# Kernel tuning notes

Hardware: AMD Instinct MI355X
Metric: run time of the kernel (lower is better)

Reference implementation:

```python
import jax, jax.numpy as jnp
import numpy as np

WH, WW = 16, 16          # window size
NUM_HEADS = 6
DIM = 192
N = WH * WW              # tokens per window

def _rel_coords_table():
    # (2*WH-1, 2*WW-1, 2), normalized and scaled by 8 (Swin-V2 style)
    rch = np.arange(-(WH - 1), WH, dtype=np.float32)
    rcw = np.arange(-(WW - 1), WW, dtype=np.float32)
    tab = np.stack(np.meshgrid(rch, rcw, indexing='ij'), axis=-1)
    tab[..., 0] /= (WH - 1)
    tab[..., 1] /= (WW - 1)
    tab *= 8.0
    return tab

def _rel_pos_index():
    # (N, N) int indices into the flattened bias table
    coords = np.stack(np.meshgrid(np.arange(WH), np.arange(WW), indexing='ij'))  # (2,WH,WW)
    cf = coords.reshape(2, -1)                                                   # (2,N)
    rel = cf[:, :, None] - cf[:, None, :]                                        # (2,N,N)
    rel = rel.transpose(1, 2, 0).astype(np.int64)                                # (N,N,2)
    rel[..., 0] += WH - 1
    rel[..., 1] += WW - 1
    rel[..., 0] *= 2 * WW - 1
    return rel.sum(-1)                                                           # (N,N)

_TABLE = jnp.asarray(_rel_coords_table())          # (2WH-1, 2WW-1, 2)
_INDEX = jnp.asarray(_rel_pos_index().reshape(-1)) # (N*N,)

def setup_inputs() -> dict:
    key = jax.random.key(0)
    ks = jax.random.split(key, 8)
    B_ = 256  # num_windows(64) * batch(4)
    return {
        'x': jax.random.normal(ks[0], (B_, N, DIM), dtype=jnp.float32),
        'scale': jax.random.uniform(ks[1], (1, 2), dtype=jnp.float32),
        'mask': jnp.zeros((64, N, N), dtype=jnp.float32),
        'qkv_w': jax.random.normal(ks[2], (3 * DIM, DIM), dtype=jnp.float32) * 0.02,
        'qkv_b': jnp.zeros((3 * DIM,), dtype=jnp.float32),
        'cpb_w1': jax.random.normal(ks[3], (512, 4), dtype=jnp.float32) * 0.02,
        'cpb_b1': jnp.zeros((512,), dtype=jnp.float32),
        'cpb_w2': jax.random.normal(ks[4], (NUM_HEADS, 512), dtype=jnp.float32) * 0.02,
        'cpb_b2': jnp.zeros((NUM_HEADS,), dtype=jnp.float32),
        'proj_w': jax.random.normal(ks[5], (DIM, DIM), dtype=jnp.float32) * 0.02,
        'proj_b': jnp.zeros((DIM,), dtype=jnp.float32),
    }

def reference(x, scale, mask, qkv_w, qkv_b, cpb_w1, cpb_b1, cpb_w2, cpb_b2, proj_w, proj_b):
    B_, n, C = x.shape
    H = NUM_HEADS
    hd = C // H
    qk_scale = hd ** -0.5

    qkv = x @ qkv_w.T + qkv_b                       # (B_, N, 3C)
    qkv = qkv.reshape(B_, n, 3, H, hd).transpose(2, 0, 3, 1, 4)
    q, k, v = qkv[0], qkv[1], qkv[2]                # each (B_, H, N, hd)

    attn = jnp.einsum('bhnd,bhmd->bhnm', q * qk_scale, k)  # (B_, H, N, N)

    # continuous relative position bias: concat table with broadcast scale -> MLP
    rel_cell = jnp.broadcast_to(scale[0], _TABLE.shape[:2] + (2,))    # (2WH-1,2WW-1,2)
    coords4 = jnp.concatenate([_TABLE, rel_cell], axis=-1)            # (...,4)
    hmid = jax.nn.relu(coords4 @ cpb_w1.T + cpb_b1)                   # (...,512)
    table = (hmid @ cpb_w2.T + cpb_b2).reshape(-1, H)                 # (M, H)
    bias = table[_INDEX].reshape(n, n, H).transpose(2, 0, 1)          # (H, N, N)

    attn = attn + bias[None]
    nW = mask.shape[0]
    attn = attn.reshape(B_ // nW, nW, H, n, n) + mask[None, :, None]
    attn = attn.reshape(B_, H, n, n)
    attn = jax.nn.softmax(attn, axis=-1)

    out = jnp.einsum('bhnm,bhmd->bhnd', attn, v)    # (B_, H, N, hd)
    out = out.transpose(0, 2, 1, 3).reshape(B_, n, C)
    return out @ proj_w.T + proj_b
```

## Files before the change

### kernel.cpp

```cpp
#include <hip/hip_runtime.h>
#include <math.h>

#define N_TOK 256
#define NHEADS 6
#define DIM_C 192
#define HD 32
#define B_WIN 256

typedef short bf16x8 __attribute__((ext_vector_type(8)));
typedef float f32x4 __attribute__((ext_vector_type(4)));

__device__ inline short f2bf(float f) {
    unsigned u = __float_as_uint(f);
    u = (u + 0x7fffu + ((u >> 16) & 1u)) >> 16;
    return (short)u;
}
__device__ inline short f2bf_fast(float f) {
    return (short)((__float_as_uint(f) + 0x8000u) >> 16);
}
__device__ inline float bf2f(short s) {
    return __uint_as_float(((unsigned)(unsigned short)s) << 16);
}

__global__ __launch_bounds__(512) void cpb_table_kernel(
    const float* __restrict__ scale, const float* __restrict__ w1,
    const float* __restrict__ b1, const float* __restrict__ w2,
    const float* __restrict__ b2, float* __restrict__ table)
{
    __shared__ float red[512];
    const int e = blockIdx.x;
    const int i = e / 31, j = e % 31;
    const float t0 = ((float)(i - 15)) * (8.0f / 15.0f);
    const float t1 = ((float)(j - 15)) * (8.0f / 15.0f);
    const float s0 = scale[0], s1 = scale[1];
    const int t = threadIdx.x;
    const float* w = w1 + t * 4;
    float h = w[0] * t0 + w[1] * t1 + w[2] * s0 + w[3] * s1 + b1[t];
    h = fmaxf(h, 0.0f);
    for (int head = 0; head < NHEADS; ++head) {
        red[t] = h * w2[head * 512 + t];
        __syncthreads();
        for (int s = 256; s > 0; s >>= 1) {
            if (t < s) red[t] += red[t + s];
            __syncthreads();
        }
        if (t == 0) table[e * NHEADS + head] = red[0] + b2[head];
        __syncthreads();
    }
}


__global__ __launch_bounds__(256) void bias_perm_kernel(
    const float* __restrict__ table, short* __restrict__ bias_p)
{
    const int idx8 = blockIdx.x * 256 + threadIdx.x;
    const int h = idx8 >> 13;
    const int rem = idx8 & 8191;
    const int rb = rem >> 9;
    const int g = (rem >> 6) & 7;
    const int lane = rem & 63;
    const int quad = lane >> 4, l15 = lane & 15;
    bf16x8 o;
#pragma unroll
    for (int j = 0; j < 8; ++j) {
        const int nt = g * 2 + (j >> 2), r = j & 3;
        const int row = rb * 16 + quad * 4 + r;
        const int col = nt * 16 + l15;
        const int rel0 = (row >> 4) - (col >> 4) + 15;
        const int rel1 = (row & 15) - (col & 15) + 15;
        o[j] = f2bf(table[(rel0 * 31 + rel1) * NHEADS + h]);
    }
    ((bf16x8*)bias_p)[idx8] = o;
}

__global__ __launch_bounds__(256) void mask_perm_kernel(
    const float* __restrict__ mask, short* __restrict__ mask_p)
{
    const int idx8 = blockIdx.x * 256 + threadIdx.x;
    const int bw = idx8 >> 13;
    const int rem = idx8 & 8191;
    const int rb = rem >> 9;
    const int g = (rem >> 6) & 7;
    const int lane = rem & 63;
    const int quad = lane >> 4, l15 = lane & 15;
    const float* ms = mask + ((size_t)bw << 16);
    bf16x8 o;
#pragma unroll
    for (int j = 0; j < 8; ++j) {
        const int nt = g * 2 + (j >> 2), r = j & 3;
        const int row = rb * 16 + quad * 4 + r;
        const int col = nt * 16 + l15;
        o[j] = f2bf(ms[row * 256 + col]);
    }
    ((bf16x8*)mask_p)[idx8] = o;
}

__global__ __launch_bounds__(256) void f32_to_bf16_kernel(
    const float* __restrict__ in, short* __restrict__ out, int n4)
{
    const int i = blockIdx.x * 256 + threadIdx.x;
    if (i < n4) {
        float4 v = ((const float4*)in)[i];
        short4 s;
        s.x = f2bf(v.x); s.y = f2bf(v.y); s.z = f2bf(v.z); s.w = f2bf(v.w);
        ((short4*)out)[i] = s;
    }
}

__global__ __launch_bounds__(256) void qkv_gemm_kernel(
    const short* __restrict__ x16, const short* __restrict__ w16,
    const float* __restrict__ qkv_b,
    short* __restrict__ qb, short* __restrict__ kb, short* __restrict__ vb)
{
    const int t = threadIdx.x;
    const int lane = t & 63;
    const int w = t >> 6;
    const int l15 = lane & 15, quad = lane >> 4;
    const int n0 = blockIdx.x * 64;
    const int m0 = blockIdx.y * 128 + w * 32;

    f32x4 acc[2][4] = {};
#pragma unroll
    for (int ks = 0; ks < 6; ++ks) {
        bf16x8 af[2];
#pragma unroll
        for (int mt = 0; mt < 2; ++mt)
            af[mt] = *(const bf16x8*)(x16 + (size_t)(m0 + mt * 16 + l15) * DIM_C + ks * 32 + quad * 8);
        bf16x8 bfr[4];
#pragma unroll
        for (int nt = 0; nt < 4; ++nt)
            bfr[nt] = *(const bf16x8*)(w16 + (size_t)(n0 + nt * 16 + l15) * DIM_C + ks * 32 + quad * 8);
#pragma unroll
        for (int mt = 0; mt < 2; ++mt)
#pragma unroll
            for (int nt = 0; nt < 4; ++nt)
                acc[mt][nt] = __builtin_amdgcn_mfma_f32_16x16x32_bf16(af[mt], bfr[nt], acc[mt][nt], 0, 0, 0);
    }

    const int which = n0 / DIM_C;
    short* outp = (which == 0) ? qb : (which == 1) ? kb : vb;
    const float qscale = (which == 0) ? 0.17677669529663689f : 1.0f;
#pragma unroll
    for (int mt = 0; mt < 2; ++mt) {
#pragma unroll
        for (int r = 0; r < 4; ++r) {
            const int m = m0 + mt * 16 + quad * 4 + r;
            const int b = m >> 8, tok = m & 255;
#pragma unroll
            for (int nt = 0; nt < 4; ++nt) {
                const int c = n0 + nt * 16 + l15;
                const int rem = c - which * DIM_C;
                const int h = rem >> 5, d = rem & 31;
                const float val = (acc[mt][nt][r] + qkv_b[c]) * qscale;
                outp[((size_t)((b * NHEADS + h) * N_TOK + tok)) * HD + d] = f2bf(val);
            }
        }
    }
}

__global__ __launch_bounds__(256) void proj_gemm_kernel(
    const short* __restrict__ A16, const short* __restrict__ w16,
    const float* __restrict__ proj_b, float* __restrict__ out)
{
    const int t = threadIdx.x;
    const int lane = t & 63;
    const int w = t >> 6;
    const int l15 = lane & 15, quad = lane >> 4;
    const int n0 = blockIdx.x * 64;
    const int m0 = blockIdx.y * 128 + w * 32;

    f32x4 acc[2][4] = {};
#pragma unroll
    for (int ks = 0; ks < 6; ++ks) {
        bf16x8 af[2];
#pragma unroll
        for (int mt = 0; mt < 2; ++mt)
            af[mt] = *(const bf16x8*)(A16 + (size_t)(m0 + mt * 16 + l15) * DIM_C + ks * 32 + quad * 8);
        bf16x8 bfr[4];
#pragma unroll
        for (int nt = 0; nt < 4; ++nt)
            bfr[nt] = *(const bf16x8*)(w16 + (size_t)(n0 + nt * 16 + l15) * DIM_C + ks * 32 + quad * 8);
#pragma unroll
        for (int mt = 0; mt < 2; ++mt)
#pragma unroll
            for (int nt = 0; nt < 4; ++nt)
                acc[mt][nt] = __builtin_amdgcn_mfma_f32_16x16x32_bf16(af[mt], bfr[nt], acc[mt][nt], 0, 0, 0);
    }

#pragma unroll
    for (int mt = 0; mt < 2; ++mt) {
#pragma unroll
        for (int r = 0; r < 4; ++r) {
            const int m = m0 + mt * 16 + quad * 4 + r;
#pragma unroll
            for (int nt = 0; nt < 4; ++nt) {
                const int c = n0 + nt * 16 + l15;
                out[(size_t)m * DIM_C + c] = acc[mt][nt][r] + proj_b[c];
            }
        }
    }
}

#define PS_LD 264

__global__ __launch_bounds__(256, 3) void attn_mfma_kernel(
    const short* __restrict__ q, const short* __restrict__ k,
    const short* __restrict__ v, const short* __restrict__ bias_p,
    const short* __restrict__ mask_p, short* __restrict__ out16)
{
    __shared__ __align__(16) short Vt[32][PS_LD];
    __shared__ __align__(16) short Pw[4][16][PS_LD];

    const int h = blockIdx.x;
    const int b = blockIdx.y;
    const int t = threadIdx.x;
    const int lane = t & 63;
    const int w = t >> 6;
    const int l15 = lane & 15;
    const int quad = lane >> 4;
    const size_t slab = ((size_t)(b * NHEADS + h)) * (N_TOK * HD);

    {
        const bf16x8* vrow = (const bf16x8*)(v + slab + (size_t)t * HD);
#pragma unroll
        for (int u = 0; u < 4; ++u) {
            bf16x8 vv = vrow[u];
#pragma unroll
            for (int j = 0; j < 8; ++j) {
                const int d = u * 8 + j;
                Vt[d][t ^ (((d >> 3) & 1) * 16)] = vv[j];
            }
        }
    }
    __syncthreads();

    const short* bslab = bias_p + h * 65536;
    const short* mslab = mask_p + ((b & 63) * 65536);

    for (int chunk = 0; chunk < 4; ++chunk) {
        const int rb = chunk * 4 + w;

        const bf16x8 qf = *(const bf16x8*)(q + slab + (size_t)(rb * 16 + l15) * HD + quad * 8);

        f32x4 S[16];
#pragma unroll
        for (int nt = 0; nt < 16; ++nt) {
            const bf16x8 kf = *(const bf16x8*)(k + slab + (size_t)(nt * 16 + l15) * HD + quad * 8);
            f32x4 z = {0.f, 0.f, 0.f, 0.f};
            S[nt] = __builtin_amdgcn_mfma_f32_16x16x32_bf16(qf, kf, z, 0, 0, 0);
        }

        float mx[4] = {-1e30f, -1e30f, -1e30f, -1e30f};
#pragma unroll
        for (int half = 0; half < 2; ++half) {
            bf16x8 bb[4], mm[4];
#pragma unroll
            for (int gg = 0; gg < 4; ++gg) {
                const int g = half * 4 + gg;
                const int off = ((rb * 8 + g) * 64 + lane) * 8;
                bb[gg] = *(const bf16x8*)(bslab + off);
                mm[gg] = *(const bf16x8*)(mslab + off);
            }
#pragma unroll
            for (int gg = 0; gg < 4; ++gg) {
#pragma unroll
                for (int jj = 0; jj < 8; ++jj) {
                    const int nt = (half * 4 + gg) * 2 + (jj >> 2);
                    const int r = jj & 3;
                    const float sv = S[nt][r] + bf2f(bb[gg][jj]) + bf2f(mm[gg][jj]);
                    S[nt][r] = sv;
                    mx[r] = fmaxf(mx[r], sv);
                }
            }
        }

#pragma unroll
        for (int r = 0; r < 4; ++r) {
            mx[r] = fmaxf(mx[r], __shfl_xor(mx[r], 1));
            mx[r] = fmaxf(mx[r], __shfl_xor(mx[r], 2));
            mx[r] = fmaxf(mx[r], __shfl_xor(mx[r], 4));
            mx[r] = fmaxf(mx[r], __shfl_xor(mx[r], 8));
        }

        float sm[4] = {0.f, 0.f, 0.f, 0.f};
#pragma unroll
        for (int nt = 0; nt < 16; ++nt) {
#pragma unroll
            for (int r = 0; r < 4; ++r) {
                const float p = __expf(S[nt][r] - mx[r]);
                sm[r] += p;
                const int lr = quad * 4 + r;
                Pw[w][lr][(nt * 16 + l15) ^ (((lr >> 3) & 1) * 16)] = f2bf_fast(p);
            }
        }
        float inv[4];
#pragma unroll
        for (int r = 0; r < 4; ++r) {
            sm[r] += __shfl_xor(sm[r], 1);
            sm[r] += __shfl_xor(sm[r], 2);
            sm[r] += __shfl_xor(sm[r], 4);
            sm[r] += __shfl_xor(sm[r], 8);
            inv[r] = __builtin_amdgcn_rcpf(sm[r]);
        }

        __asm__ volatile("s_waitcnt lgkmcnt(0)" ::: "memory");

        f32x4 O0 = {0.f, 0.f, 0.f, 0.f};
        f32x4 O1 = {0.f, 0.f, 0.f, 0.f};
        const int sw = ((l15 >> 3) & 1) * 16;
#pragma unroll
        for (int ks = 0; ks < 8; ++ks) {
            const int cb = ks * 32 + quad * 8;
            bf16x8 af  = *(const bf16x8*)&Pw[w][l15][cb ^ sw];
            bf16x8 bf0 = *(const bf16x8*)&Vt[l15][cb ^ sw];
            bf16x8 bf1 = *(const bf16x8*)&Vt[16 + l15][cb ^ sw];
            O0 = __builtin_amdgcn_mfma_f32_16x16x32_bf16(af, bf0, O0, 0, 0, 0);
            O1 = __builtin_amdgcn_mfma_f32_16x16x32_bf16(af, bf1, O1, 0, 0, 0);
        }

#pragma unroll
        for (int r = 0; r < 4; ++r) {
            const int token = rb * 16 + quad * 4 + r;
            short* dst = out16 + ((size_t)(b * N_TOK + token)) * DIM_C + h * HD;
            dst[l15]      = f2bf_fast(O0[r] * inv[r]);
            dst[16 + l15] = f2bf_fast(O1[r] * inv[r]);
        }
    }
}

extern "C" void kernel_launch(void* const* d_in, const int* in_sizes, int n_in,
                              void* d_out, int out_size, void* d_ws, size_t ws_size,
                              hipStream_t stream)
{
    const float* x      = (const float*)d_in[0];
    const float* scale  = (const float*)d_in[1];
    const float* mask   = (const float*)d_in[2];
    const float* qkv_w  = (const float*)d_in[3];
    const float* qkv_b  = (const float*)d_in[4];
    const float* cpb_w1 = (const float*)d_in[5];
    const float* cpb_b1 = (const float*)d_in[6];
    const float* cpb_w2 = (const float*)d_in[7];
    const float* cpb_b2 = (const float*)d_in[8];
    const float* proj_w = (const float*)d_in[9];
    const float* proj_b = (const float*)d_in[10];
    float* out = (float*)d_out;

    const size_t per = (size_t)B_WIN * NHEADS * N_TOK * HD;
    short* wss     = (short*)d_ws;
    short* qb      = wss;
    short* kb      = qb + per;
    short* vb      = kb + per;
    short* ao      = vb + per;
    short* x16     = ao + per;
    short* bias_p  = x16 + per;
    short* mask_p  = bias_p + 393216;
    short* qkvw16  = mask_p + 4194304;
    short* projw16 = qkvw16 + 110592;
    float* table   = (float*)(projw16 + 36864);

    cpb_table_kernel<<<961, 512, 0, stream>>>(scale, cpb_w1, cpb_b1, cpb_w2, cpb_b2, table);

    bias_perm_kernel<<<(NHEADS * 8192) / 256, 256, 0, stream>>>(table, bias_p);
    mask_perm_kernel<<<(64 * 8192) / 256, 256, 0, stream>>>(mask, mask_p);

    f32_to_bf16_kernel<<<(int)((per / 4 + 255) / 256), 256, 0, stream>>>(x, x16, (int)(per / 4));
    f32_to_bf16_kernel<<<(110592 / 4 + 255) / 256, 256, 0, stream>>>(qkv_w, qkvw16, 110592 / 4);
    f32_to_bf16_kernel<<<(36864 / 4 + 255) / 256, 256, 0, stream>>>(proj_w, projw16, 36864 / 4);

    qkv_gemm_kernel<<<dim3(9, 512), 256, 0, stream>>>(x16, qkvw16, qkv_b, qb, kb, vb);

    attn_mfma_kernel<<<dim3(NHEADS, B_WIN), 256, 0, stream>>>(qb, kb, vb, bias_p, mask_p, ao);

    proj_gemm_kernel<<<dim3(3, 512), 256, 0, stream>>>(ao, projw16, proj_b, out);
}
```

Measured before the change: 361.8 us.

## Hoist K fragments, fold bias+mask into MFMA accumulator, remap blocks for mask reuse

The attention kernel now loads all 16 K fragments into registers once per block instead of once per row chunk. The bias and mask sum is passed as the MFMA accumulator input, which removes a separate add pass. The grid is flattened, and blocks are remapped so that consecutive blocks share the same mask window across heads and batches, which should improve L2 reuse. The cost is higher register pressure from holding 16 K fragments, which may lower occupancy under launch_bounds(256,3).

```diff
diff --git a/kernel.cpp b/kernel.cpp
--- a/kernel.cpp
+++ b/kernel.cpp
@@ -211,8 +211,13 @@
     __shared__ __align__(16) short Vt[32][PS_LD];
     __shared__ __align__(16) short Pw[4][16][PS_LD];
 
-    const int h = blockIdx.x;
-    const int b = blockIdx.y;
+    const int l = blockIdx.x;
+    const int s = l >> 3;
+    const int bw = (l & 7) + 8 * (s / 24);
+    const int j = s % 24;
+    const int h = j % 6;
+    const int b = (j / 6) * 64 + bw;
+
     const int t = threadIdx.x;
     const int lane = t & 63;
     const int w = t >> 6;
@@ -226,16 +231,22 @@
         for (int u = 0; u < 4; ++u) {
             bf16x8 vv = vrow[u];
 #pragma unroll
-            for (int j = 0; j < 8; ++j) {
-                const int d = u * 8 + j;
-                Vt[d][t ^ (((d >> 3) & 1) * 16)] = vv[j];
-            }
-        }
-    }
+            for (int jj = 0; jj < 8; ++jj) {
+                const int d = u * 8 + jj;
+                Vt[d][t ^ (((d >> 3) & 1) * 16)] = vv[jj];
+            }
+        }
+    }
+
+    bf16x8 kfr[16];
+#pragma unroll
+    for (int nt = 0; nt < 16; ++nt)
+        kfr[nt] = *(const bf16x8*)(k + slab + (size_t)(nt * 16 + l15) * HD + quad * 8);
+
     __syncthreads();
 
     const short* bslab = bias_p + h * 65536;
-    const short* mslab = mask_p + ((b & 63) * 65536);
+    const short* mslab = mask_p + bw * 65536;
 
     for (int chunk = 0; chunk < 4; ++chunk) {
         const int rb = chunk * 4 + w;
@@ -243,14 +254,6 @@
         const bf16x8 qf = *(const bf16x8*)(q + slab + (size_t)(rb * 16 + l15) * HD + quad * 8);
 
         f32x4 S[16];
-#pragma unroll
-        for (int nt = 0; nt < 16; ++nt) {
-            const bf16x8 kf = *(const bf16x8*)(k + slab + (size_t)(nt * 16 + l15) * HD + quad * 8);
-            f32x4 z = {0.f, 0.f, 0.f, 0.f};
-            S[nt] = __builtin_amdgcn_mfma_f32_16x16x32_bf16(qf, kf, z, 0, 0, 0);
-        }
-
-        float mx[4] = {-1e30f, -1e30f, -1e30f, -1e30f};
 #pragma unroll
         for (int half = 0; half < 2; ++half) {
             bf16x8 bb[4], mm[4];
@@ -263,17 +266,24 @@
             }
 #pragma unroll
             for (int gg = 0; gg < 4; ++gg) {
-#pragma unroll
-                for (int jj = 0; jj < 8; ++jj) {
-                    const int nt = (half * 4 + gg) * 2 + (jj >> 2);
-                    const int r = jj & 3;
-                    const float sv = S[nt][r] + bf2f(bb[gg][jj]) + bf2f(mm[gg][jj]);
-                    S[nt][r] = sv;
-                    mx[r] = fmaxf(mx[r], sv);
+                const int g = half * 4 + gg;
+                f32x4 c0, c1;
+#pragma unroll
+                for (int r = 0; r < 4; ++r) {
+                    c0[r] = bf2f(bb[gg][r])     + bf2f(mm[gg][r]);
+                    c1[r] = bf2f(bb[gg][4 + r]) + bf2f(mm[gg][4 + r]);
                 }
-            }
-        }
-
+                S[g * 2]     = __builtin_amdgcn_mfma_f32_16x16x32_bf16(qf, kfr[g * 2],     c0, 0, 0, 0);
+                S[g * 2 + 1] = __builtin_amdgcn_mfma_f32_16x16x32_bf16(qf, kfr[g * 2 + 1], c1, 0, 0, 0);
+            }
+        }
+
+        float mx[4] = {-1e30f, -1e30f, -1e30f, -1e30f};
+#pragma unroll
+        for (int nt = 0; nt < 16; ++nt)
+#pragma unroll
+            for (int r = 0; r < 4; ++r)
+                mx[r] = fmaxf(mx[r], S[nt][r]);
 #pragma unroll
         for (int r = 0; r < 4; ++r) {
             mx[r] = fmaxf(mx[r], __shfl_xor(mx[r], 1));
@@ -369,7 +379,7 @@
 
     qkv_gemm_kernel<<<dim3(9, 512), 256, 0, stream>>>(x16, qkvw16, qkv_b, qb, kb, vb);
 
-    attn_mfma_kernel<<<dim3(NHEADS, B_WIN), 256, 0, stream>>>(qb, kb, vb, bias_p, mask_p, ao);
+    attn_mfma_kernel<<<NHEADS * B_WIN, 256, 0, stream>>>(qb, kb, vb, bias_p, mask_p, ao);
 
     proj_gemm_kernel<<<dim3(3, 512), 256, 0, stream>>>(ao, projw16, proj_b, out);
 }
```

New measurement: 330.7 us. 8.6% less time.
